# Performance work log

Hardware: AMD Instinct MI355X
Metric: run time of the kernel (lower is better)

Reference implementation:

```python
import jax, jax.numpy as jnp
import numpy as np

E = 256            # embedding_dim
S = 16             # num_surv_samples
N = 8192           # batch of events
NUM_NODES = 20000  # max_dst_idx - min_src_idx + 1
N_SRC = 10000
MIN_DST = 10000
TD_HR_MAX = 5000.0


def setup_inputs() -> dict:
    key = jax.random.key(0)
    ks = jax.random.split(key, 16)
    all_embeddings = jax.random.normal(ks[0], (NUM_NODES, E), dtype=jnp.float32)
    assoc = jnp.arange(NUM_NODES, dtype=jnp.int64 if jax.config.jax_enable_x64 else jnp.int32)
    src = jax.random.randint(ks[1], (N,), 0, N_SRC)
    pos_dst = jax.random.randint(ks[2], (N,), 0, N_SRC) + MIN_DST
    last_update = jax.random.uniform(ks[3], (NUM_NODES,), dtype=jnp.float32) * 1000.0
    last_time_pos = jax.random.uniform(ks[4], (N,), dtype=jnp.float32) * 1000.0
    cur_time = 2000.0 + jax.random.uniform(ks[5], (N,), dtype=jnp.float32) * 100.0
    u_non_embeddings = jax.random.normal(ks[6], (S * N, E), dtype=jnp.float32)
    v_non_embeddings = jax.random.normal(ks[7], (S * N, E), dtype=jnp.float32)
    td_surv_step = jax.random.uniform(ks[8], (S, N), dtype=jnp.float32)
    event_inten_accu = jax.random.uniform(ks[9], (N_SRC, N_SRC), dtype=jnp.float32)
    W_omega = jax.random.normal(ks[10], (1, 2 * E), dtype=jnp.float32) * (1.0 / np.sqrt(2 * E))
    b_omega = jax.random.normal(ks[11], (1,), dtype=jnp.float32) * 0.01
    psi = 0.5 * jnp.ones((1,), dtype=jnp.float32)
    alpha = jax.random.uniform(ks[12], (1,), dtype=jnp.float32)
    w_t = jax.random.uniform(ks[13], (1,), dtype=jnp.float32)
    return dict(all_embeddings=all_embeddings, assoc=assoc, src=src, pos_dst=pos_dst,
                last_update=last_update, cur_time=cur_time,
                u_non_embeddings=u_non_embeddings, v_non_embeddings=v_non_embeddings,
                last_time_pos=last_time_pos, td_surv_step=td_surv_step,
                event_inten_accu=event_inten_accu, W_omega=W_omega, b_omega=b_omega,
                psi=psi, alpha=alpha, w_t=w_t)


def _hawkes_intensity(z_u, z_v, td, W, b, psi, alpha, w_t):
    # symmetric=False path of hawkes_intensity_singleType
    Wu, Wv = W[0, :E], W[0, E:]          # split Linear over [z_u; z_v] concat
    g = z_u @ Wu + z_v @ Wv + b[0]       # [M]
    td_norm = td / TD_HR_MAX
    g = g + alpha[0] * jnp.exp(-w_t[0] * td_norm)
    g_psi = jnp.clip(g / (psi[0] + 1e-7), -75.0, 75.0)
    return psi[0] * (jnp.log1p(jnp.exp(-g_psi)) + g_psi)


def reference(all_embeddings, assoc, src, pos_dst, last_update, cur_time,
              u_non_embeddings, v_non_embeddings, last_time_pos, td_surv_step,
              event_inten_accu, W_omega, b_omega, psi, alpha, w_t):
    z_src = all_embeddings[assoc[src]]
    z_dst = all_embeddings[assoc[pos_dst]]
    lu_src = last_update[assoc[src]]
    lu_dst = last_update[assoc[pos_dst]]

    td_pos = cur_time - last_time_pos  # (unused downstream on this branch)
    last_update_max = jnp.maximum(lu_src, lu_dst)
    use_accu = (last_time_pos >= last_update_max).astype(jnp.float32)
    t_uv = jnp.maximum(last_update_max, last_time_pos)
    td_uv = cur_time - t_uv

    # unit_sampling=False: Monte-Carlo survival samples
    td_uv_non = td_surv_step * td_uv[None, :]          # [S, N]

    lambda_uv = _hawkes_intensity(z_src, z_dst, td_uv, W_omega, b_omega, psi, alpha, w_t)
    lambda_surv = _hawkes_intensity(u_non_embeddings, v_non_embeddings,
                                    td_uv_non.reshape(-1), W_omega, b_omega,
                                    psi, alpha, w_t).reshape(S, N)

    integral = jnp.mean(lambda_surv, axis=0) * td_uv \
        + use_accu * event_inten_accu[src, pos_dst - MIN_DST]
    loss_surv = jnp.sum(integral)
    loss_lambda = -jnp.sum(jnp.log(lambda_uv + 1e-7))

    n = z_src.shape[0]
    return (loss_lambda / n, loss_surv / n)
```

## Files before the change

### kernel.cpp

```cpp
#include <hip/hip_runtime.h>

constexpr int   S_    = 16;
constexpr int   N_    = 8192;
constexpr int   NSRC  = 10000;
constexpr int   MINDST= 10000;
constexpr float TDMAX = 5000.0f;

__device__ __forceinline__ float wave_reduce_sum(float v) {
#pragma unroll
    for (int off = 32; off > 0; off >>= 1)
        v += __shfl_xor(v, off, 64);
    return v;
}

__device__ __forceinline__ float hawkes(float gdot, float td,
                                        float b, float psi, float alpha, float wt) {
    float g  = gdot + b + alpha * expf(-wt * (td * (1.0f / TDMAX)));
    float gp = g / (psi + 1e-7f);
    gp = fminf(fmaxf(gp, -75.0f), 75.0f);
    return psi * (log1pf(expf(-gp)) + gp);
}

__global__ __launch_bounds__(256) void decoder_tp_fused(
    const float* __restrict__ emb,
    const int*   __restrict__ assoc,
    const int*   __restrict__ src,
    const int*   __restrict__ dst,
    const float* __restrict__ last_update,
    const float* __restrict__ cur_time,
    const float* __restrict__ u_non,
    const float* __restrict__ v_non,
    const float* __restrict__ last_time_pos,
    const float* __restrict__ td_step,
    const float* __restrict__ accu,
    const float* __restrict__ W,
    const float* __restrict__ b_p,
    const float* __restrict__ psi_p,
    const float* __restrict__ alpha_p,
    const float* __restrict__ wt_p,
    float* __restrict__ out)
{
    const int wave = threadIdx.x >> 6;
    const int lane = threadIdx.x & 63;
    const int i    = (blockIdx.x << 2) + wave;

    const float4* __restrict__ W4 = (const float4*)W;
    const float4 wu = W4[lane];
    const float4 wv = W4[64 + lane];
    const float b0    = b_p[0];
    const float psi   = psi_p[0];
    const float alpha = alpha_p[0];
    const float wt    = wt_p[0];

    const int si = src[i];
    const int di = dst[i];
    const int as = assoc[si];
    const int ad = assoc[di];
    const float lum  = fmaxf(last_update[as], last_update[ad]);
    const float ltp  = last_time_pos[i];
    const float ct   = cur_time[i];
    const float t_uv = fmaxf(lum, ltp);
    const float td_uv = ct - t_uv;

    const float4* __restrict__ Z4 = (const float4*)emb;
    const float4 zs = Z4[(size_t)as * 64 + lane];
    const float4 zd = Z4[(size_t)ad * 64 + lane];
    float d = zs.x * wu.x + zs.y * wu.y + zs.z * wu.z + zs.w * wu.w
            + zd.x * wv.x + zd.y * wv.y + zd.z * wv.z + zd.w * wv.w;
    d = wave_reduce_sum(d);
    const float lam_uv = hawkes(d, td_uv, b0, psi, alpha, wt);
    const float loss_lambda = -logf(lam_uv + 1e-7f);

    const float4* __restrict__ U4 = (const float4*)u_non;
    const float4* __restrict__ V4 = (const float4*)v_non;
    float lam_sum = 0.0f;
#pragma unroll 4
    for (int s = 0; s < S_; ++s) {
        const size_t p = (size_t)s * N_ + i;
        const float4 uu = U4[p * 64 + lane];
        const float4 vv = V4[p * 64 + lane];
        float dd = uu.x * wu.x + uu.y * wu.y + uu.z * wu.z + uu.w * wu.w
                 + vv.x * wv.x + vv.y * wv.y + vv.z * wv.z + vv.w * wv.w;
        dd = wave_reduce_sum(dd);
        lam_sum += hawkes(dd, td_step[p] * td_uv, b0, psi, alpha, wt);
    }
    float loss_surv = lam_sum * (1.0f / S_) * td_uv;
    if (ltp >= lum)
        loss_surv += accu[(size_t)si * NSRC + (di - MINDST)];

    __shared__ float s_ll[4], s_sv[4];
    if (lane == 0) { s_ll[wave] = loss_lambda; s_sv[wave] = loss_surv; }
    __syncthreads();
    if (threadIdx.x == 0) {
        const float a = s_ll[0] + s_ll[1] + s_ll[2] + s_ll[3];
        const float c = s_sv[0] + s_sv[1] + s_sv[2] + s_sv[3];
        atomicAdd(&out[0], a * (1.0f / N_));
        atomicAdd(&out[1], c * (1.0f / N_));
    }
}

extern "C" void kernel_launch(void* const* d_in, const int* in_sizes, int n_in,
                              void* d_out, int out_size, void* d_ws, size_t ws_size,
                              hipStream_t stream) {
    const float* emb           = (const float*)d_in[0];
    const int*   assoc         = (const int*)  d_in[1];
    const int*   src           = (const int*)  d_in[2];
    const int*   dst           = (const int*)  d_in[3];
    const float* last_update   = (const float*)d_in[4];
    const float* cur_time      = (const float*)d_in[5];
    const float* u_non         = (const float*)d_in[6];
    const float* v_non         = (const float*)d_in[7];
    const float* last_time_pos = (const float*)d_in[8];
    const float* td_step       = (const float*)d_in[9];
    const float* accu          = (const float*)d_in[10];
    const float* W             = (const float*)d_in[11];
    const float* b_p           = (const float*)d_in[12];
    const float* psi_p         = (const float*)d_in[13];
    const float* alpha_p       = (const float*)d_in[14];
    const float* wt_p          = (const float*)d_in[15];
    float* out = (float*)d_out;

    hipMemsetAsync(out, 0, 2 * sizeof(float), stream);

    decoder_tp_fused<<<N_ / 4, 256, 0, stream>>>(
        emb, assoc, src, dst, last_update, cur_time, u_non, v_non,
        last_time_pos, td_step, accu, W, b_p, psi_p, alpha_p, wt_p, out);
}
```

Measured before the change: 637.5 us.

## Use nontemporal streaming loads, hoist accu gather, and two-stage reduction

Loads the large u/v sample rows with nontemporal hints so the one-pass stream does not pollute the cache. The scattered event_inten_accu gather is issued early so its latency overlaps the other work. The global float atomics and memset are replaced by per-block partials in workspace plus a second single-block reduction kernel, with the atomic path kept as a fallback. This adds a second kernel launch in exchange for removing the atomics.

```diff
diff --git a/kernel.cpp b/kernel.cpp
--- a/kernel.cpp
+++ b/kernel.cpp
@@ -1,10 +1,12 @@
 #include <hip/hip_runtime.h>
 
-constexpr int   S_    = 16;
-constexpr int   N_    = 8192;
-constexpr int   NSRC  = 10000;
-constexpr int   MINDST= 10000;
-constexpr float TDMAX = 5000.0f;
+constexpr int   S_     = 16;
+constexpr int   N_     = 8192;
+constexpr int   NSRC   = 10000;
+constexpr int   MINDST = 10000;
+constexpr float TDMAX  = 5000.0f;
+
+typedef float f4 __attribute__((ext_vector_type(4)));
 
 __device__ __forceinline__ float wave_reduce_sum(float v) {
 #pragma unroll
@@ -21,7 +23,8 @@
     return psi * (log1pf(expf(-gp)) + gp);
 }
 
-__global__ __launch_bounds__(256) void decoder_tp_fused(
+template <bool USE_ATOMIC>
+__global__ __launch_bounds__(256) void decoder_stage1(
     const float* __restrict__ emb,
     const int*   __restrict__ assoc,
     const int*   __restrict__ src,
@@ -38,15 +41,16 @@
     const float* __restrict__ psi_p,
     const float* __restrict__ alpha_p,
     const float* __restrict__ wt_p,
-    float* __restrict__ out)
+    float2* __restrict__ partial,
+    float*  __restrict__ out)
 {
     const int wave = threadIdx.x >> 6;
     const int lane = threadIdx.x & 63;
     const int i    = (blockIdx.x << 2) + wave;
 
-    const float4* __restrict__ W4 = (const float4*)W;
-    const float4 wu = W4[lane];
-    const float4 wv = W4[64 + lane];
+    const f4* __restrict__ W4 = (const f4*)W;
+    const f4 wu = W4[lane];
+    const f4 wv = W4[64 + lane];
     const float b0    = b_p[0];
     const float psi   = psi_p[0];
     const float alpha = alpha_p[0];
@@ -56,37 +60,37 @@
     const int di = dst[i];
     const int as = assoc[si];
     const int ad = assoc[di];
+    const float accu_v = accu[(size_t)si * NSRC + (di - MINDST)];
     const float lum  = fmaxf(last_update[as], last_update[ad]);
     const float ltp  = last_time_pos[i];
     const float ct   = cur_time[i];
     const float t_uv = fmaxf(lum, ltp);
     const float td_uv = ct - t_uv;
 
-    const float4* __restrict__ Z4 = (const float4*)emb;
-    const float4 zs = Z4[(size_t)as * 64 + lane];
-    const float4 zd = Z4[(size_t)ad * 64 + lane];
+    const f4* __restrict__ Z4 = (const f4*)emb;
+    const f4 zs = Z4[(size_t)as * 64 + lane];
+    const f4 zd = Z4[(size_t)ad * 64 + lane];
     float d = zs.x * wu.x + zs.y * wu.y + zs.z * wu.z + zs.w * wu.w
             + zd.x * wv.x + zd.y * wv.y + zd.z * wv.z + zd.w * wv.w;
     d = wave_reduce_sum(d);
     const float lam_uv = hawkes(d, td_uv, b0, psi, alpha, wt);
     const float loss_lambda = -logf(lam_uv + 1e-7f);
 
-    const float4* __restrict__ U4 = (const float4*)u_non;
-    const float4* __restrict__ V4 = (const float4*)v_non;
+    const f4* __restrict__ U4 = (const f4*)u_non;
+    const f4* __restrict__ V4 = (const f4*)v_non;
     float lam_sum = 0.0f;
 #pragma unroll 4
     for (int s = 0; s < S_; ++s) {
         const size_t p = (size_t)s * N_ + i;
-        const float4 uu = U4[p * 64 + lane];
-        const float4 vv = V4[p * 64 + lane];
+        const f4 uu = __builtin_nontemporal_load(&U4[p * 64 + lane]);
+        const f4 vv = __builtin_nontemporal_load(&V4[p * 64 + lane]);
         float dd = uu.x * wu.x + uu.y * wu.y + uu.z * wu.z + uu.w * wu.w
                  + vv.x * wv.x + vv.y * wv.y + vv.z * wv.z + vv.w * wv.w;
         dd = wave_reduce_sum(dd);
         lam_sum += hawkes(dd, td_step[p] * td_uv, b0, psi, alpha, wt);
     }
     float loss_surv = lam_sum * (1.0f / S_) * td_uv;
-    if (ltp >= lum)
-        loss_surv += accu[(size_t)si * NSRC + (di - MINDST)];
+    if (ltp >= lum) loss_surv += accu_v;
 
     __shared__ float s_ll[4], s_sv[4];
     if (lane == 0) { s_ll[wave] = loss_lambda; s_sv[wave] = loss_surv; }
@@ -94,8 +98,34 @@
     if (threadIdx.x == 0) {
         const float a = s_ll[0] + s_ll[1] + s_ll[2] + s_ll[3];
         const float c = s_sv[0] + s_sv[1] + s_sv[2] + s_sv[3];
-        atomicAdd(&out[0], a * (1.0f / N_));
-        atomicAdd(&out[1], c * (1.0f / N_));
+        if (USE_ATOMIC) {
+            atomicAdd(&out[0], a * (1.0f / N_));
+            atomicAdd(&out[1], c * (1.0f / N_));
+        } else {
+            float2 pr; pr.x = a; pr.y = c;
+            partial[blockIdx.x] = pr;
+        }
+    }
+}
+
+__global__ __launch_bounds__(256) void decoder_stage2(
+    const float2* __restrict__ partial, float* __restrict__ out)
+{
+    float a = 0.0f, c = 0.0f;
+    for (int k = threadIdx.x; k < N_ / 4; k += 256) {
+        const float2 q = partial[k];
+        a += q.x; c += q.y;
+    }
+    a = wave_reduce_sum(a);
+    c = wave_reduce_sum(c);
+    __shared__ float sa[4], sc[4];
+    const int wave = threadIdx.x >> 6;
+    const int lane = threadIdx.x & 63;
+    if (lane == 0) { sa[wave] = a; sc[wave] = c; }
+    __syncthreads();
+    if (threadIdx.x == 0) {
+        out[0] = (sa[0] + sa[1] + sa[2] + sa[3]) * (1.0f / N_);
+        out[1] = (sc[0] + sc[1] + sc[2] + sc[3]) * (1.0f / N_);
     }
 }
 
@@ -120,9 +150,19 @@
     const float* wt_p          = (const float*)d_in[15];
     float* out = (float*)d_out;
 
-    hipMemsetAsync(out, 0, 2 * sizeof(float), stream);
-
-    decoder_tp_fused<<<N_ / 4, 256, 0, stream>>>(
-        emb, assoc, src, dst, last_update, cur_time, u_non, v_non,
-        last_time_pos, td_step, accu, W, b_p, psi_p, alpha_p, wt_p, out);
+    const size_t need = (size_t)(N_ / 4) * sizeof(float2);
+    if (d_ws != nullptr && ws_size >= need) {
+        float2* partial = (float2*)d_ws;
+        decoder_stage1<false><<<N_ / 4, 256, 0, stream>>>(
+            emb, assoc, src, dst, last_update, cur_time, u_non, v_non,
+            last_time_pos, td_step, accu, W, b_p, psi_p, alpha_p, wt_p,
+            partial, out);
+        decoder_stage2<<<1, 256, 0, stream>>>(partial, out);
+    } else {
+        hipMemsetAsync(out, 0, 2 * sizeof(float), stream);
+        decoder_stage1<true><<<N_ / 4, 256, 0, stream>>>(
+            emb, assoc, src, dst, last_update, cur_time, u_non, v_non,
+            last_time_pos, td_step, accu, W, b_p, psi_p, alpha_p, wt_p,
+            nullptr, out);
+    }
 }
```

After: 612.3 us. -4.0%, faster.
